# Kernel optimization log

Hardware: AMD Instinct MI355X
Metric: run time of the kernel (lower is better)

## Reference

```python
import jax, jax.numpy as jnp
import numpy as np

N_NODES = 50000
N_EDGES = 800000
N_GRAPHS = 512
HIDDEN = 256
NODE_FEAT = 9
LAYERS = 4


def setup_inputs() -> dict:
    key = jax.random.key(0)
    ks = jax.random.split(key, 9)
    x = jax.random.normal(ks[0], (N_NODES, NODE_FEAT), dtype=jnp.float32)
    edge_index = jax.random.randint(ks[1], (2, N_EDGES), 0, N_NODES, dtype=jnp.int64)
    batch = jnp.sort(jax.random.randint(ks[2], (N_NODES,), 0, N_GRAPHS, dtype=jnp.int64))
    embed_W = jax.random.normal(ks[3], (NODE_FEAT, HIDDEN), dtype=jnp.float32) * (1.0 / np.sqrt(NODE_FEAT))
    embed_b = jnp.zeros((HIDDEN,), dtype=jnp.float32)
    conv_W = jax.random.normal(ks[4], (LAYERS, HIDDEN, HIDDEN), dtype=jnp.float32) * (1.0 / np.sqrt(HIDDEN))
    conv_b = jnp.zeros((LAYERS, HIDDEN), dtype=jnp.float32)
    out_W = jax.random.normal(ks[5], (HIDDEN, 1), dtype=jnp.float32) * (1.0 / np.sqrt(HIDDEN))
    out_b = jnp.zeros((1,), dtype=jnp.float32)
    return {"x": x, "edge_index": edge_index, "batch": batch,
            "embed_W": embed_W, "embed_b": embed_b,
            "conv_W": conv_W, "conv_b": conv_b,
            "out_W": out_W, "out_b": out_b}


def reference(x, edge_index, batch, embed_W, embed_b, conv_W, conv_b, out_W, out_b):
    n = x.shape[0]
    src, dst = edge_index[0], edge_index[1]
    # GCN symmetric normalization with self-loops: deg includes the self-loop (+1)
    deg = jax.ops.segment_sum(jnp.ones(src.shape[0], x.dtype), dst, num_segments=n) + 1.0
    dinv = jax.lax.rsqrt(deg)                       # [N]
    norm_e = dinv[src] * dinv[dst]                  # [E] edge coefficient
    self_coef = (dinv * dinv)[:, None]              # [N,1] self-loop coefficient

    h = jax.nn.relu(x @ embed_W + embed_b)          # [N,H]
    for l in range(conv_W.shape[0]):
        hw = h @ conv_W[l]                          # [N,H] transform first
        msg = hw[src] * norm_e[:, None]             # [E,H] gather + scale
        agg = jax.ops.segment_sum(msg, dst, num_segments=n)  # scatter-add
        agg = agg + hw * self_coef                  # self-loop contribution
        h = jax.nn.relu(agg + conv_b[l])

    # global mean pool over graph ids
    sums = jax.ops.segment_sum(h, batch, num_segments=N_GRAPHS)           # [G,H]
    cnt = jax.ops.segment_sum(jnp.ones(n, h.dtype), batch, num_segments=N_GRAPHS)
    pooled = sums / jnp.maximum(cnt, 1.0)[:, None]
    return pooled @ out_W + out_b                   # [G,1]
```

## Files before the change

kernel.cpp:

```cpp
#include <hip/hip_runtime.h>

#define N_NODES 50000
#define N_EDGES 800000
#define N_GRAPHS 512
#define HIDDEN 256
#define NODE_FEAT 9
#define LAYERS 4
#define BUCKET 64

typedef float floatx4 __attribute__((ext_vector_type(4)));
typedef short short8 __attribute__((ext_vector_type(8)));
typedef unsigned uint2v __attribute__((ext_vector_type(2)));

__device__ __forceinline__ float bf2f(unsigned u) {
    unsigned v = u << 16;
    float f;
    __builtin_memcpy(&f, &v, 4);
    return f;
}
__device__ __forceinline__ unsigned short f2bf(float f) {
    unsigned v;
    __builtin_memcpy(&v, &f, 4);
    v += 0x7FFFu + ((v >> 16) & 1u);
    return (unsigned short)(v >> 16);
}

__global__ void fillb_kernel(const int* __restrict__ src, const int* __restrict__ dst,
                             int* __restrict__ cnt, int* __restrict__ col_src, int E) {
    int e = blockIdx.x * blockDim.x + threadIdx.x;
    if (e < E) {
        int d = dst[e];
        int pos = atomicAdd(&cnt[d], 1);
        if (pos < BUCKET) col_src[d * BUCKET + pos] = src[e];
    }
}

__global__ void dinv_kernel(const int* __restrict__ cnt, float* __restrict__ dinv, int N) {
    int i = blockIdx.x * blockDim.x + threadIdx.x;
    if (i < N) dinv[i] = rsqrtf((float)(cnt[i] + 1));
}

__global__ void findstart_kernel(const int* __restrict__ batch, int* __restrict__ gstart) {
    int g = blockIdx.x * blockDim.x + threadIdx.x;
    if (g > N_GRAPHS) return;
    if (g == N_GRAPHS) { gstart[g] = N_NODES; return; }
    int lo = 0, hi = N_NODES;
    while (lo < hi) {
        int mid = (lo + hi) >> 1;
        if (batch[mid] < g) lo = mid + 1; else hi = mid;
    }
    gstart[g] = lo;
}

__global__ __launch_bounds__(256) void packW_kernel(const float* __restrict__ W,
                                                    unsigned short* __restrict__ Wsw) {
    int idx = blockIdx.x * 256 + threadIdx.x;
    int lane = idx & 63;
    int ct   = (idx >> 6) & 15;
    int ks   = (idx >> 10) & 7;
    int l    = idx >> 13;
    int n = ct * 16 + (lane & 15);
    int kbase = ks * 32 + (lane >> 4) * 8;
    const float* Wl = W + (size_t)l * HIDDEN * HIDDEN;
    alignas(16) unsigned short tmp[8];
    #pragma unroll
    for (int j = 0; j < 8; j++)
        tmp[j] = f2bf(Wl[(size_t)(kbase + j) * HIDDEN + n]);
    *(uint4*)&Wsw[(size_t)idx * 8] = *(const uint4*)tmp;
}

__global__ __launch_bounds__(256, 2) void embed_gemm(const float* __restrict__ x,
                                                     const float* __restrict__ embW,
                                                     const float* __restrict__ embb,
                                                     const unsigned short* __restrict__ Wsw,
                                                     unsigned short* __restrict__ hwout, int N) {
    __shared__ unsigned short As[64][264];
    int t = threadIdx.x;
    int wv = t >> 6, lane = t & 63, quad = lane >> 4, l15 = lane & 15;
    int n0 = blockIdx.x * 64;

    const short8* Wl = (const short8*)Wsw;
    short8 bq[3][4];
    #pragma unroll
    for (int p = 0; p < 2; p++)
        #pragma unroll
        for (int ci = 0; ci < 4; ci++)
            bq[p][ci] = Wl[(size_t)(p * 16 + wv * 4 + ci) * 64 + lane];

    #pragma unroll 2
    for (int i = 0; i < 8; i++) {
        int j = t + i * 256;
        int r = j >> 5;
        int c8 = j & 31;
        int n = n0 + r;
        unsigned o0 = 0, o1 = 0, o2 = 0, o3 = 0;
        if (n < N) {
            float xr[NODE_FEAT];
            #pragma unroll
            for (int k = 0; k < NODE_FEAT; k++) xr[k] = x[(size_t)n * NODE_FEAT + k];
            float4 a0 = *(const float4*)&embb[c8 * 8];
            float4 a1 = *(const float4*)&embb[c8 * 8 + 4];
            #pragma unroll
            for (int k = 0; k < NODE_FEAT; k++) {
                float4 w0 = *(const float4*)&embW[k * HIDDEN + c8 * 8];
                float4 w1 = *(const float4*)&embW[k * HIDDEN + c8 * 8 + 4];
                a0.x += xr[k] * w0.x; a0.y += xr[k] * w0.y;
                a0.z += xr[k] * w0.z; a0.w += xr[k] * w0.w;
                a1.x += xr[k] * w1.x; a1.y += xr[k] * w1.y;
                a1.z += xr[k] * w1.z; a1.w += xr[k] * w1.w;
            }
            o0 = (unsigned)f2bf(fmaxf(a0.x, 0.f)) | ((unsigned)f2bf(fmaxf(a0.y, 0.f)) << 16);
            o1 = (unsigned)f2bf(fmaxf(a0.z, 0.f)) | ((unsigned)f2bf(fmaxf(a0.w, 0.f)) << 16);
            o2 = (unsigned)f2bf(fmaxf(a1.x, 0.f)) | ((unsigned)f2bf(fmaxf(a1.y, 0.f)) << 16);
            o3 = (unsigned)f2bf(fmaxf(a1.z, 0.f)) | ((unsigned)f2bf(fmaxf(a1.w, 0.f)) << 16);
        }
        *(uint4*)&As[r][c8 * 8] = make_uint4(o0, o1, o2, o3);
    }
    __syncthreads();

    floatx4 acc[4][4];
    #pragma unroll
    for (int i = 0; i < 4; i++)
        #pragma unroll
        for (int j = 0; j < 4; j++)
            acc[i][j] = (floatx4){0.f, 0.f, 0.f, 0.f};

    #pragma unroll
    for (int ks = 0; ks < 8; ks++) {
        if (ks < 6) {
            #pragma unroll
            for (int ci = 0; ci < 4; ci++)
                bq[(ks + 2) % 3][ci] = Wl[(size_t)((ks + 2) * 16 + wv * 4 + ci) * 64 + lane];
        }
        short8 a[4];
        #pragma unroll
        for (int rt = 0; rt < 4; rt++)
            a[rt] = *(const short8*)&As[rt * 16 + l15][ks * 32 + quad * 8];
        #pragma unroll
        for (int rt = 0; rt < 4; rt++)
            #pragma unroll
            for (int ci = 0; ci < 4; ci++)
                acc[rt][ci] = __builtin_amdgcn_mfma_f32_16x16x32_bf16(a[rt], bq[ks % 3][ci], acc[rt][ci], 0, 0, 0);
    }

    __syncthreads();
    #pragma unroll
    for (int rt = 0; rt < 4; rt++) {
        #pragma unroll
        for (int ci = 0; ci < 4; ci++) {
            int col = (wv * 4 + ci) * 16 + l15;
            int rowb = rt * 16 + quad * 4;
            #pragma unroll
            for (int reg = 0; reg < 4; reg++)
                As[rowb + reg][col] = f2bf(acc[rt][ci][reg]);
        }
    }
    __syncthreads();
    #pragma unroll
    for (int i = 0; i < 8; i++) {
        int j = t + i * 256;
        int r = j >> 5;
        int c = j & 31;
        int n = n0 + r;
        if (n < N)
            *(uint4*)&hwout[(size_t)n * HIDDEN + c * 8] = *(const uint4*)&As[r][c * 8];
    }
}

__global__ __launch_bounds__(256, 2) void gemm_mfma(const unsigned short* __restrict__ hin,
                                                    const unsigned short* __restrict__ Wsw,
                                                    unsigned short* __restrict__ hwout, int N) {
    __shared__ unsigned short As[64][264];
    int t = threadIdx.x;
    int wv = t >> 6, lane = t & 63, quad = lane >> 4, l15 = lane & 15;
    int n0 = blockIdx.x * 64;
    const uint4* h4 = (const uint4*)hin;

    uint4 av[8];
    #pragma unroll
    for (int i = 0; i < 8; i++) {
        int j = t + i * 256;
        int r = j >> 5;
        int c = j & 31;
        int n = n0 + r;
        av[i] = make_uint4(0u, 0u, 0u, 0u);
        if (n < N) av[i] = h4[(size_t)n * 32 + c];
    }
    const short8* Wl = (const short8*)Wsw;
    short8 bq[3][4];
    #pragma unroll
    for (int p = 0; p < 2; p++)
        #pragma unroll
        for (int ci = 0; ci < 4; ci++)
            bq[p][ci] = Wl[(size_t)(p * 16 + wv * 4 + ci) * 64 + lane];
    #pragma unroll
    for (int i = 0; i < 8; i++) {
        int j = t + i * 256;
        int r = j >> 5;
        int c = j & 31;
        *(uint4*)&As[r][c * 8] = av[i];
    }
    __syncthreads();

    floatx4 acc[4][4];
    #pragma unroll
    for (int i = 0; i < 4; i++)
        #pragma unroll
        for (int j = 0; j < 4; j++)
            acc[i][j] = (floatx4){0.f, 0.f, 0.f, 0.f};

    #pragma unroll
    for (int ks = 0; ks < 8; ks++) {
        if (ks < 6) {
            #pragma unroll
            for (int ci = 0; ci < 4; ci++)
                bq[(ks + 2) % 3][ci] = Wl[(size_t)((ks + 2) * 16 + wv * 4 + ci) * 64 + lane];
        }
        short8 a[4];
        #pragma unroll
        for (int rt = 0; rt < 4; rt++)
            a[rt] = *(const short8*)&As[rt * 16 + l15][ks * 32 + quad * 8];
        #pragma unroll
        for (int rt = 0; rt < 4; rt++)
            #pragma unroll
            for (int ci = 0; ci < 4; ci++)
                acc[rt][ci] = __builtin_amdgcn_mfma_f32_16x16x32_bf16(a[rt], bq[ks % 3][ci], acc[rt][ci], 0, 0, 0);
    }

    __syncthreads();
    #pragma unroll
    for (int rt = 0; rt < 4; rt++) {
        #pragma unroll
        for (int ci = 0; ci < 4; ci++) {
            int col = (wv * 4 + ci) * 16 + l15;
            int rowb = rt * 16 + quad * 4;
            #pragma unroll
            for (int reg = 0; reg < 4; reg++)
                As[rowb + reg][col] = f2bf(acc[rt][ci][reg]);
        }
    }
    __syncthreads();
    #pragma unroll
    for (int i = 0; i < 8; i++) {
        int j = t + i * 256;
        int r = j >> 5;
        int c = j & 31;
        int n = n0 + r;
        if (n < N)
            *(uint4*)&hwout[(size_t)n * HIDDEN + c * 8] = *(const uint4*)&As[r][c * 8];
    }
}

__global__ __launch_bounds__(256) void agg_kernel(const unsigned short* __restrict__ hw,
                                                  const int* __restrict__ cnt,
                                                  const int* __restrict__ col_src,
                                                  const float* __restrict__ dinv,
                                                  const float* __restrict__ bias,
                                                  unsigned short* __restrict__ hout) {
    __shared__ uint2 sEdge[4][64];
    int wv = threadIdx.x >> 6, lane = threadIdx.x & 63;
    int n = blockIdx.x * 4 + wv;
    if (n >= N_NODES) return;
    float dn = dinv[n];
    int deg = cnt[n]; if (deg > BUCKET) deg = BUCKET;

    uint2 s2 = ((const uint2*)(hw + (size_t)n * HIDDEN))[lane];
    float4 b4 = *(const float4*)&bias[4 * lane];
    float selfc = dn * dn;
    float a0 = bf2f(s2.x & 0xFFFFu) * selfc + b4.x;
    float a1 = bf2f(s2.x >> 16)     * selfc + b4.y;
    float a2 = bf2f(s2.y & 0xFFFFu) * selfc + b4.z;
    float a3 = bf2f(s2.y >> 16)     * selfc + b4.w;

    if (lane < deg) {
        int s = col_src[n * BUCKET + lane];
        float nr = dinv[s] * dn;
        unsigned nrb;
        __builtin_memcpy(&nrb, &nr, 4);
        sEdge[wv][lane] = make_uint2((unsigned)s, nrb);
    }
    for (int i = 0; i < deg; i++) {
        uint2 p = sEdge[wv][i];
        float nr;
        __builtin_memcpy(&nr, &p.y, 4);
        uint2 u = ((const uint2*)(hw + (size_t)p.x * HIDDEN))[lane];
        a0 += nr * bf2f(u.x & 0xFFFFu);
        a1 += nr * bf2f(u.x >> 16);
        a2 += nr * bf2f(u.y & 0xFFFFu);
        a3 += nr * bf2f(u.y >> 16);
    }
    unsigned p0 = (unsigned)f2bf(fmaxf(a0, 0.0f)) | ((unsigned)f2bf(fmaxf(a1, 0.0f)) << 16);
    unsigned p1 = (unsigned)f2bf(fmaxf(a2, 0.0f)) | ((unsigned)f2bf(fmaxf(a3, 0.0f)) << 16);
    uint2v pv; pv.x = p0; pv.y = p1;
    __builtin_nontemporal_store(pv, (uint2v*)(hout + (size_t)n * HIDDEN) + lane);
}

__global__ __launch_bounds__(256) void agg_dot_kernel(const unsigned short* __restrict__ hw,
                                                      const int* __restrict__ cnt,
                                                      const int* __restrict__ col_src,
                                                      const float* __restrict__ dinv,
                                                      const float* __restrict__ bias,
                                                      const float* __restrict__ outW,
                                                      float* __restrict__ dotv) {
    __shared__ uint2 sEdge[4][64];
    int wv = threadIdx.x >> 6, lane = threadIdx.x & 63;
    int n = blockIdx.x * 4 + wv;
    if (n >= N_NODES) return;
    float dn = dinv[n];
    int deg = cnt[n]; if (deg > BUCKET) deg = BUCKET;

    uint2 s2 = ((const uint2*)(hw + (size_t)n * HIDDEN))[lane];
    float4 b4 = *(const float4*)&bias[4 * lane];
    float selfc = dn * dn;
    float a0 = bf2f(s2.x & 0xFFFFu) * selfc + b4.x;
    float a1 = bf2f(s2.x >> 16)     * selfc + b4.y;
    float a2 = bf2f(s2.y & 0xFFFFu) * selfc + b4.z;
    float a3 = bf2f(s2.y >> 16)     * selfc + b4.w;

    if (lane < deg) {
        int s = col_src[n * BUCKET + lane];
        float nr = dinv[s] * dn;
        unsigned nrb;
        __builtin_memcpy(&nrb, &nr, 4);
        sEdge[wv][lane] = make_uint2((unsigned)s, nrb);
    }
    for (int i = 0; i < deg; i++) {
        uint2 p = sEdge[wv][i];
        float nr;
        __builtin_memcpy(&nr, &p.y, 4);
        uint2 u = ((const uint2*)(hw + (size_t)p.x * HIDDEN))[lane];
        a0 += nr * bf2f(u.x & 0xFFFFu);
        a1 += nr * bf2f(u.x >> 16);
        a2 += nr * bf2f(u.y & 0xFFFFu);
        a3 += nr * bf2f(u.y >> 16);
    }
    float4 w = *(const float4*)&outW[4 * lane];
    float dot = fmaxf(a0, 0.0f) * w.x + fmaxf(a1, 0.0f) * w.y
              + fmaxf(a2, 0.0f) * w.z + fmaxf(a3, 0.0f) * w.w;
    #pragma unroll
    for (int off = 32; off > 0; off >>= 1) dot += __shfl_xor(dot, off, 64);
    if (lane == 0) dotv[n] = dot;
}

__global__ __launch_bounds__(64) void finalize_kernel(const float* __restrict__ dotv,
                                                      const int* __restrict__ gstart,
                                                      const float* __restrict__ outb,
                                                      float* __restrict__ out) {
    int g = blockIdx.x;
    int lane = threadIdx.x;
    int s = gstart[g], e = gstart[g + 1];
    float acc = 0.0f;
    for (int n = s + lane; n < e; n += 64) acc += dotv[n];
    #pragma unroll
    for (int off = 32; off > 0; off >>= 1) acc += __shfl_xor(acc, off, 64);
    if (lane == 0) out[g] = acc / fmaxf((float)(e - s), 1.0f) + outb[0];
}

extern "C" void kernel_launch(void* const* d_in, const int* in_sizes, int n_in,
                              void* d_out, int out_size, void* d_ws, size_t ws_size,
                              hipStream_t stream) {
    const float* x     = (const float*)d_in[0];
    const int*   edge  = (const int*)d_in[1];
    const int*   src   = edge;
    const int*   dst   = edge + N_EDGES;
    const int*   batch = (const int*)d_in[2];
    const float* embW  = (const float*)d_in[3];
    const float* embb  = (const float*)d_in[4];
    const float* convW = (const float*)d_in[5];
    const float* convb = (const float*)d_in[6];
    const float* outW  = (const float*)d_in[7];
    const float* outb  = (const float*)d_in[8];
    float* out = (float*)d_out;

    char* ws = (char*)d_ws;
    size_t off = 0;
    auto take = [&](size_t bytes) { char* p = ws + off; off += (bytes + 255) & ~(size_t)255; return p; };
    int*   cnt     = (int*)  take((size_t)N_NODES * 4);
    int*   col_src = (int*)  take((size_t)N_NODES * BUCKET * 4);
    float* dinv    = (float*)take((size_t)N_NODES * 4);
    int*   gstart  = (int*)  take((size_t)(N_GRAPHS + 1) * 4);
    float* dotv    = (float*)take((size_t)N_NODES * 4);
    unsigned short* Wsw = (unsigned short*)take((size_t)LAYERS * 8 * 16 * 64 * 8 * 2);
    unsigned short* h0  = (unsigned short*)take((size_t)N_NODES * HIDDEN * 2);
    unsigned short* h1  = (unsigned short*)take((size_t)N_NODES * HIDDEN * 2);

    hipMemsetAsync(cnt, 0, (size_t)N_NODES * 4, stream);

    fillb_kernel<<<(N_EDGES + 255) / 256, 256, 0, stream>>>(src, dst, cnt, col_src, N_EDGES);
    dinv_kernel<<<(N_NODES + 255) / 256, 256, 0, stream>>>(cnt, dinv, N_NODES);
    findstart_kernel<<<3, 256, 0, stream>>>(batch, gstart);
    packW_kernel<<<128, 256, 0, stream>>>(convW, Wsw);

    int nblk = (N_NODES + 63) / 64;
    int ablk = (N_NODES + 3) / 4;

    embed_gemm<<<nblk, 256, 0, stream>>>(x, embW, embb, Wsw, h1, N_NODES);
    agg_kernel<<<ablk, 256, 0, stream>>>(h1, cnt, col_src, dinv, convb + 0 * HIDDEN, h0);
    gemm_mfma<<<nblk, 256, 0, stream>>>(h0, Wsw + (size_t)1 * 65536, h1, N_NODES);
    agg_kernel<<<ablk, 256, 0, stream>>>(h1, cnt, col_src, dinv, convb + 1 * HIDDEN, h0);
    gemm_mfma<<<nblk, 256, 0, stream>>>(h0, Wsw + (size_t)2 * 65536, h1, N_NODES);
    agg_kernel<<<ablk, 256, 0, stream>>>(h1, cnt, col_src, dinv, convb + 2 * HIDDEN, h0);
    gemm_mfma<<<nblk, 256, 0, stream>>>(h0, Wsw + (size_t)3 * 65536, h1, N_NODES);
    agg_dot_kernel<<<ablk, 256, 0, stream>>>(h1, cnt, col_src, dinv, convb + 3 * HIDDEN, outW, dotv);

    finalize_kernel<<<N_GRAPHS, 64, 0, stream>>>(dotv, gstart, outb, out);
}
```

Measured before the change: 436.0 us.

## Fuse edge bucketing into embed GEMM, merge aux kernels, raise GEMM occupancy

The edge-bucketing fill now runs as a grid-stride loop at the tail of the embed GEMM kernel, and the dinv and graph-start kernels are merged into one aux kernel launched afterwards. This removes two kernel launches and overlaps atomic scatter work with the GEMM tail. Both GEMM kernels also switch from triple to double buffering of the weight fragments and raise launch bounds to 3 blocks per SM, which lowers register pressure in exchange for less prefetch distance.

```diff
diff --git a/kernel.cpp b/kernel.cpp
--- a/kernel.cpp
+++ b/kernel.cpp
@@ -25,31 +25,22 @@
     return (unsigned short)(v >> 16);
 }
 
-__global__ void fillb_kernel(const int* __restrict__ src, const int* __restrict__ dst,
-                             int* __restrict__ cnt, int* __restrict__ col_src, int E) {
-    int e = blockIdx.x * blockDim.x + threadIdx.x;
-    if (e < E) {
-        int d = dst[e];
-        int pos = atomicAdd(&cnt[d], 1);
-        if (pos < BUCKET) col_src[d * BUCKET + pos] = src[e];
-    }
-}
-
-__global__ void dinv_kernel(const int* __restrict__ cnt, float* __restrict__ dinv, int N) {
-    int i = blockIdx.x * blockDim.x + threadIdx.x;
-    if (i < N) dinv[i] = rsqrtf((float)(cnt[i] + 1));
-}
-
-__global__ void findstart_kernel(const int* __restrict__ batch, int* __restrict__ gstart) {
-    int g = blockIdx.x * blockDim.x + threadIdx.x;
-    if (g > N_GRAPHS) return;
-    if (g == N_GRAPHS) { gstart[g] = N_NODES; return; }
-    int lo = 0, hi = N_NODES;
-    while (lo < hi) {
-        int mid = (lo + hi) >> 1;
-        if (batch[mid] < g) lo = mid + 1; else hi = mid;
-    }
-    gstart[g] = lo;
+__global__ __launch_bounds__(256) void aux_kernel(const int* __restrict__ cnt,
+                                                  float* __restrict__ dinv,
+                                                  const int* __restrict__ batch,
+                                                  int* __restrict__ gstart) {
+    int i = blockIdx.x * 256 + threadIdx.x;
+    if (i < N_NODES) dinv[i] = rsqrtf((float)(cnt[i] + 1));
+    int g = i - N_NODES;
+    if (g >= 0 && g <= N_GRAPHS) {
+        if (g == N_GRAPHS) { gstart[g] = N_NODES; return; }
+        int lo = 0, hi = N_NODES;
+        while (lo < hi) {
+            int mid = (lo + hi) >> 1;
+            if (batch[mid] < g) lo = mid + 1; else hi = mid;
+        }
+        gstart[g] = lo;
+    }
 }
 
 __global__ __launch_bounds__(256) void packW_kernel(const float* __restrict__ W,
@@ -69,23 +60,25 @@
     *(uint4*)&Wsw[(size_t)idx * 8] = *(const uint4*)tmp;
 }
 
-__global__ __launch_bounds__(256, 2) void embed_gemm(const float* __restrict__ x,
+__global__ __launch_bounds__(256, 3) void embed_gemm(const float* __restrict__ x,
                                                      const float* __restrict__ embW,
                                                      const float* __restrict__ embb,
                                                      const unsigned short* __restrict__ Wsw,
-                                                     unsigned short* __restrict__ hwout, int N) {
+                                                     unsigned short* __restrict__ hwout, int N,
+                                                     const int* __restrict__ srcE,
+                                                     const int* __restrict__ dstE,
+                                                     int* __restrict__ cnt,
+                                                     int* __restrict__ col_src) {
     __shared__ unsigned short As[64][264];
     int t = threadIdx.x;
     int wv = t >> 6, lane = t & 63, quad = lane >> 4, l15 = lane & 15;
     int n0 = blockIdx.x * 64;
 
     const short8* Wl = (const short8*)Wsw;
-    short8 bq[3][4];
-    #pragma unroll
-    for (int p = 0; p < 2; p++)
-        #pragma unroll
-        for (int ci = 0; ci < 4; ci++)
-            bq[p][ci] = Wl[(size_t)(p * 16 + wv * 4 + ci) * 64 + lane];
+    short8 bq[2][4];
+    #pragma unroll
+    for (int ci = 0; ci < 4; ci++)
+        bq[0][ci] = Wl[(size_t)(wv * 4 + ci) * 64 + lane];
 
     #pragma unroll 2
     for (int i = 0; i < 8; i++) {
@@ -127,10 +120,10 @@
 
     #pragma unroll
     for (int ks = 0; ks < 8; ks++) {
-        if (ks < 6) {
+        if (ks < 7) {
             #pragma unroll
             for (int ci = 0; ci < 4; ci++)
-                bq[(ks + 2) % 3][ci] = Wl[(size_t)((ks + 2) * 16 + wv * 4 + ci) * 64 + lane];
+                bq[(ks + 1) & 1][ci] = Wl[(size_t)((ks + 1) * 16 + wv * 4 + ci) * 64 + lane];
         }
         short8 a[4];
         #pragma unroll
@@ -140,7 +133,7 @@
         for (int rt = 0; rt < 4; rt++)
             #pragma unroll
             for (int ci = 0; ci < 4; ci++)
-                acc[rt][ci] = __builtin_amdgcn_mfma_f32_16x16x32_bf16(a[rt], bq[ks % 3][ci], acc[rt][ci], 0, 0, 0);
+                acc[rt][ci] = __builtin_amdgcn_mfma_f32_16x16x32_bf16(a[rt], bq[ks & 1][ci], acc[rt][ci], 0, 0, 0);
     }
 
     __syncthreads();
@@ -165,9 +158,16 @@
         if (n < N)
             *(uint4*)&hwout[(size_t)n * HIDDEN + c * 8] = *(const uint4*)&As[r][c * 8];
     }
-}
-
-__global__ __launch_bounds__(256, 2) void gemm_mfma(const unsigned short* __restrict__ hin,
+
+    int stride = gridDim.x * 256;
+    for (int e = blockIdx.x * 256 + t; e < N_EDGES; e += stride) {
+        int d = dstE[e];
+        int pos = atomicAdd(&cnt[d], 1);
+        if (pos < BUCKET) col_src[d * BUCKET + pos] = srcE[e];
+    }
+}
+
+__global__ __launch_bounds__(256, 3) void gemm_mfma(const unsigned short* __restrict__ hin,
                                                     const unsigned short* __restrict__ Wsw,
                                                     unsigned short* __restrict__ hwout, int N) {
     __shared__ unsigned short As[64][264];
@@ -187,12 +187,10 @@
         if (n < N) av[i] = h4[(size_t)n * 32 + c];
     }
     const short8* Wl = (const short8*)Wsw;
-    short8 bq[3][4];
-    #pragma unroll
-    for (int p = 0; p < 2; p++)
-        #pragma unroll
-        for (int ci = 0; ci < 4; ci++)
-            bq[p][ci] = Wl[(size_t)(p * 16 + wv * 4 + ci) * 64 + lane];
+    short8 bq[2][4];
+    #pragma unroll
+    for (int ci = 0; ci < 4; ci++)
+        bq[0][ci] = Wl[(size_t)(wv * 4 + ci) * 64 + lane];
     #pragma unroll
     for (int i = 0; i < 8; i++) {
         int j = t + i * 256;
@@ -211,10 +209,10 @@
 
     #pragma unroll
     for (int ks = 0; ks < 8; ks++) {
-        if (ks < 6) {
+        if (ks < 7) {
             #pragma unroll
             for (int ci = 0; ci < 4; ci++)
-                bq[(ks + 2) % 3][ci] = Wl[(size_t)((ks + 2) * 16 + wv * 4 + ci) * 64 + lane];
+                bq[(ks + 1) & 1][ci] = Wl[(size_t)((ks + 1) * 16 + wv * 4 + ci) * 64 + lane];
         }
         short8 a[4];
         #pragma unroll
@@ -224,7 +222,7 @@
         for (int rt = 0; rt < 4; rt++)
             #pragma unroll
             for (int ci = 0; ci < 4; ci++)
-                acc[rt][ci] = __builtin_amdgcn_mfma_f32_16x16x32_bf16(a[rt], bq[ks % 3][ci], acc[rt][ci], 0, 0, 0);
+                acc[rt][ci] = __builtin_amdgcn_mfma_f32_16x16x32_bf16(a[rt], bq[ks & 1][ci], acc[rt][ci], 0, 0, 0);
     }
 
     __syncthreads();
@@ -386,15 +384,15 @@
 
     hipMemsetAsync(cnt, 0, (size_t)N_NODES * 4, stream);
 
-    fillb_kernel<<<(N_EDGES + 255) / 256, 256, 0, stream>>>(src, dst, cnt, col_src, N_EDGES);
-    dinv_kernel<<<(N_NODES + 255) / 256, 256, 0, stream>>>(cnt, dinv, N_NODES);
-    findstart_kernel<<<3, 256, 0, stream>>>(batch, gstart);
     packW_kernel<<<128, 256, 0, stream>>>(convW, Wsw);
 
     int nblk = (N_NODES + 63) / 64;
     int ablk = (N_NODES + 3) / 4;
-
-    embed_gemm<<<nblk, 256, 0, stream>>>(x, embW, embb, Wsw, h1, N_NODES);
+    int xblk = (N_NODES + N_GRAPHS + 1 + 255) / 256;
+
+    embed_gemm<<<nblk, 256, 0, stream>>>(x, embW, embb, Wsw, h1, N_NODES,
+                                         src, dst, cnt, col_src);
+    aux_kernel<<<xblk, 256, 0, stream>>>(cnt, dinv, batch, gstart);
     agg_kernel<<<ablk, 256, 0, stream>>>(h1, cnt, col_src, dinv, convb + 0 * HIDDEN, h0);
     gemm_mfma<<<nblk, 256, 0, stream>>>(h0, Wsw + (size_t)1 * 65536, h1, N_NODES);
     agg_kernel<<<ablk, 256, 0, stream>>>(h1, cnt, col_src, dinv, convb + 1 * HIDDEN, h0);
```

After: 465.9 us. +6.9%, slower.
